# Optimization experiments

Measured on AMD Instinct MI355X. Metric: run time of the kernel, lower is better.

The kernel has to match this reference:

```python
import jax, jax.numpy as jnp
import numpy as np

N, E, D, H, C, ED = 50000, 800000, 128, 4, 32, 1
EFF = H * C  # 128 == D, so residual proj is Identity
FFN_H = 2 * EFF


def setup_inputs() -> dict:
    key = jax.random.key(0)
    ks = jax.random.split(key, 16)
    def p(k, shape, fan_in):
        return jax.random.normal(k, shape, dtype=jnp.float32) / np.sqrt(fan_in)
    return {
        "x": jax.random.normal(ks[0], (N, D), dtype=jnp.float32),
        "edge_attr": jax.random.normal(ks[1], (E, ED), dtype=jnp.float32),
        "W_l": p(ks[2], (D, EFF), D),
        "b_l": jnp.zeros((EFF,), jnp.float32),
        "W_r": p(ks[3], (D, EFF), D),
        "b_r": jnp.zeros((EFF,), jnp.float32),
        "W_e": p(ks[4], (ED, EFF), ED),
        "att": p(ks[5], (H, C), C),
        "bias_out": jnp.zeros((EFF,), jnp.float32),
        "W_gate": p(ks[6], (EFF, 1), EFF),
        "b_gate": jnp.zeros((1,), jnp.float32),
        "W_ffn1": p(ks[7], (EFF, FFN_H), EFF),
        "b_ffn1": jnp.zeros((FFN_H,), jnp.float32),
        "W_ffn2": p(ks[8], (FFN_H, EFF), FFN_H),
        "b_ffn2": jnp.zeros((EFF,), jnp.float32),
        "ln_gamma": jnp.ones((EFF,), jnp.float32),
        "ln_beta": jnp.zeros((EFF,), jnp.float32),
        "edge_index": jax.random.randint(ks[9], (2, E), 0, N, dtype=jnp.int32),
    }


def _gat_block(x, edge_attr, W_l, b_l, W_r, b_r, W_e, att, bias_out,
               W_gate, b_gate, W_ffn1, b_ffn1, W_ffn2, b_ffn2,
               ln_gamma, ln_beta, edge_index):
    n = x.shape[0]
    # add self loops (PyG default), edge_attr filled with mean
    loop = jnp.arange(n, dtype=edge_index.dtype)
    src = jnp.concatenate([edge_index[0], loop])
    dst = jnp.concatenate([edge_index[1], loop])
    ea = jnp.concatenate([edge_attr,
                          jnp.broadcast_to(edge_attr.mean(0, keepdims=True), (n, edge_attr.shape[1]))])
    # GATv2: separate source/target transforms + edge embedding
    xl = (x @ W_l + b_l).reshape(n, H, C)   # source features
    xr = (x @ W_r + b_r).reshape(n, H, C)   # target features
    ee = (ea @ W_e).reshape(-1, H, C)
    xj = xl[src]                             # [Et,H,C]
    m = jax.nn.leaky_relu(xj + xr[dst] + ee, negative_slope=0.2)
    logits = jnp.einsum('ehc,hc->eh', m, att)           # [Et,H]
    # segment softmax over destination nodes
    mx = jax.ops.segment_max(logits, dst, num_segments=n)
    ex = jnp.exp(logits - mx[dst])
    den = jax.ops.segment_sum(ex, dst, num_segments=n)
    alpha = ex / den[dst]
    out = jax.ops.segment_sum(xj * alpha[..., None], dst, num_segments=n)
    out = out.reshape(n, EFF) + bias_out
    # block: ELU, gated residual (proj is Identity since D==EFF), FFN, LayerNorm
    h = jax.nn.elu(out)
    gate = jax.nn.sigmoid(h @ W_gate + b_gate)
    y = gate * h + (1.0 - gate) * x
    ffn = jax.nn.relu(y @ W_ffn1 + b_ffn1) @ W_ffn2 + b_ffn2
    y = y + ffn
    mu = y.mean(-1, keepdims=True)
    var = y.var(-1, keepdims=True)
    y = (y - mu) * jax.lax.rsqrt(var + 1e-5) * ln_gamma + ln_beta
    return y  # dropout is identity in eval mode


def reference(x, edge_attr, W_l, b_l, W_r, b_r, W_e, att, bias_out,
              W_gate, b_gate, W_ffn1, b_ffn1, W_ffn2, b_ffn2,
              ln_gamma, ln_beta, edge_index):
    return _gat_block(x, edge_attr, W_l, b_l, W_r, b_r, W_e, att, bias_out,
                      W_gate, b_gate, W_ffn1, b_ffn1, W_ffn2, b_ffn2,
                      ln_gamma, ln_beta, edge_index)
```

## Files before the change

kernel.cpp:

```cpp
#include <hip/hip_runtime.h>
#include <hip/hip_bf16.h>

#define NODES 50000
#define NEDGE 800000
#define ETOT  850000

#define NRANGE 49
#define SB 256
#define ES ((ETOT + SB - 1) / SB)

#define XF_TILES 1563
#define HIST_BLKS 256
#define FUSE_GRID (2 * HIST_BLKS + (XF_TILES - HIST_BLKS))

typedef __hip_bfloat16 bf16;
typedef __attribute__((ext_vector_type(8))) short bf16x8;
typedef __attribute__((ext_vector_type(4))) float f32x4;

__device__ __forceinline__ bf16 f2bf(float v) { return __float2bfloat16(v); }
__device__ __forceinline__ float bflo(unsigned int v) { return __uint_as_float(v << 16); }
__device__ __forceinline__ float bfhi(unsigned int v) { return __uint_as_float(v & 0xffff0000u); }

__device__ __forceinline__ unsigned int pack2(float a, float b) {
    bf16 x = f2bf(a), y = f2bf(b);
    unsigned short xs = *reinterpret_cast<unsigned short*>(&x);
    unsigned short ys = *reinterpret_cast<unsigned short*>(&y);
    return ((unsigned int)ys << 16) | (unsigned int)xs;
}

__device__ __forceinline__ unsigned short bfbits(float v) {
    bf16 x = f2bf(v);
    return *reinterpret_cast<unsigned short*>(&x);
}

__device__ __forceinline__ void hilo(float v, unsigned short& h, unsigned short& l) {
    h = bfbits(v);
    float hv = __uint_as_float((unsigned int)h << 16);
    l = bfbits(v - hv);
}

__device__ __forceinline__ void split8(const float* v, bf16x8& hi, bf16x8& lo) {
    #pragma unroll
    for (int e = 0; e < 8; ++e) {
        unsigned short hb, lb;
        hilo(v[e], hb, lb);
        ((short*)&hi)[e] = (short)hb;
        ((short*)&lo)[e] = (short)lb;
    }
}

__global__ __launch_bounds__(256) void k_wx(const float* W_l, const float* W_r,
                                            const float* W1, const float* W2,
                                            bf16* wlh, bf16* wll,
                                            bf16* wrh, bf16* wrl,
                                            bf16* w1h, bf16* w1l,
                                            bf16* w2h, bf16* w2l) {
    int tid = blockIdx.x * blockDim.x + threadIdx.x;
    unsigned short h, l;
    if (tid < 32768) {
        int m = tid >> 14, t = tid & 16383;
        int c = t >> 7, k = t & 127;
        hilo((m ? W_r : W_l)[k * 128 + c], h, l);
        (m ? wrh : wlh)[t] = *(bf16*)&h;
        (m ? wrl : wll)[t] = *(bf16*)&l;
    } else if (tid < 65536) {
        int t = tid - 32768;
        int c = t >> 7, k = t & 127;
        hilo(W1[k * 256 + c], h, l);
        w1h[t] = *(bf16*)&h;
        w1l[t] = *(bf16*)&l;
    } else {
        int t = tid - 65536;
        int c = t >> 8, k = t & 255;
        hilo(W2[k * 128 + c], h, l);
        w2h[t] = *(bf16*)&h;
        w2l[t] = *(bf16*)&l;
    }
}

__global__ __launch_bounds__(256) void k_fuse(const float* edge_attr, const int* ei,
                                              float* sum_ea, int* rhist,
                                              const float* x,
                                              const bf16* wlh, const bf16* wll,
                                              const bf16* wrh, const bf16* wrl,
                                              const float* b_l, const float* b_r,
                                              bf16* xl, bf16* xr) {
    __shared__ __align__(16) float s_x[32][132];
    const int bid = blockIdx.x;
    int idx;
    bool isprep;
    if (bid < 2 * HIST_BLKS) { isprep = (bid & 1); idx = bid >> 1; }
    else { isprep = false; idx = HIST_BLKS + (bid - 2 * HIST_BLKS); }

    if (isprep) {
        int* hcnt = (int*)&s_x[0][0];
        const int t = threadIdx.x;
        if (t < 64) hcnt[t] = 0;
        __syncthreads();
        const int e0 = idx * ES;
        int e1 = e0 + ES; if (e1 > ETOT) e1 = ETOT;
        float local = 0.f;
        for (int e = e0 + t; e < e1; e += 256) {
            int dst = (e < NEDGE) ? ei[NEDGE + e] : (e - NEDGE);
            atomicAdd(&hcnt[dst >> 10], 1);
            if (e < NEDGE) local += edge_attr[e];
        }
        #pragma unroll
        for (int s = 1; s < 64; s <<= 1) local += __shfl_xor(local, s, 64);
        if ((t & 63) == 0) atomicAdd(sum_ea, local);
        __syncthreads();
        if (t < 64) rhist[idx * 64 + t] = hcnt[t];
        return;
    }

    const int tid = threadIdx.x;
    const int n0 = idx * 32;
    for (int it = 0; it < 4; ++it) {
        int idx4 = (it * 256 + tid) * 4;
        int n = idx4 >> 7, j = idx4 & 127;
        int node = n0 + n;
        float4 v = make_float4(0.f, 0.f, 0.f, 0.f);
        if (node < NODES) v = *(const float4*)(x + node * 128 + j);
        *(float4*)&s_x[n][j] = v;
    }
    __syncthreads();

    const int wv4  = tid >> 6;
    const int ln   = tid & 63;
    const int lrow = ln & 15;
    const int lk8  = (ln >> 4) << 3;
    const int m    = wv4 >> 1;
    const int cb   = (wv4 & 1) * 64;
    const bf16* Bh = m ? wrh : wlh;
    const bf16* Bl = m ? wrl : wll;
    const float* bias = m ? b_r : b_l;

    f32x4 acc[2][4];
    #pragma unroll
    for (int mt = 0; mt < 2; ++mt)
        #pragma unroll
        for (int i = 0; i < 4; ++i)
            acc[mt][i] = (f32x4){0.f, 0.f, 0.f, 0.f};
    #pragma unroll
    for (int kk = 0; kk < 4; ++kk) {
        int k0 = kk * 32 + lk8;
        float a0f[8], a1f[8];
        *(float4*)&a0f[0] = *(const float4*)&s_x[lrow][k0];
        *(float4*)&a0f[4] = *(const float4*)&s_x[lrow][k0 + 4];
        *(float4*)&a1f[0] = *(const float4*)&s_x[16 + lrow][k0];
        *(float4*)&a1f[4] = *(const float4*)&s_x[16 + lrow][k0 + 4];
        bf16x8 a0h, a0l, a1h, a1l;
        split8(a0f, a0h, a0l);
        split8(a1f, a1h, a1l);
        #pragma unroll
        for (int i = 0; i < 4; ++i) {
            int col = cb + (i << 4) + lrow;
            bf16x8 bh = *(const bf16x8*)(Bh + col * 128 + k0);
            bf16x8 bl = *(const bf16x8*)(Bl + col * 128 + k0);
            acc[0][i] = __builtin_amdgcn_mfma_f32_16x16x32_bf16(a0l, bh, acc[0][i], 0, 0, 0);
            acc[0][i] = __builtin_amdgcn_mfma_f32_16x16x32_bf16(a0h, bl, acc[0][i], 0, 0, 0);
            acc[0][i] = __builtin_amdgcn_mfma_f32_16x16x32_bf16(a0h, bh, acc[0][i], 0, 0, 0);
            acc[1][i] = __builtin_amdgcn_mfma_f32_16x16x32_bf16(a1l, bh, acc[1][i], 0, 0, 0);
            acc[1][i] = __builtin_amdgcn_mfma_f32_16x16x32_bf16(a1h, bl, acc[1][i], 0, 0, 0);
            acc[1][i] = __builtin_amdgcn_mfma_f32_16x16x32_bf16(a1h, bh, acc[1][i], 0, 0, 0);
        }
    }
    __syncthreads();
    bf16* s_o = (bf16*)&s_x[0][0];
    #pragma unroll
    for (int mt = 0; mt < 2; ++mt) {
        #pragma unroll
        for (int i = 0; i < 4; ++i) {
            int colg = cb + (i << 4) + lrow;
            float bv = bias[colg];
            #pragma unroll
            for (int r = 0; r < 4; ++r) {
                int row = (mt << 4) + ((ln >> 4) << 2) + r;
                s_o[row * 264 + m * 136 + colg] = f2bf(acc[mt][i][r] + bv);
            }
        }
    }
    __syncthreads();
    #pragma unroll
    for (int rep = 0; rep < 2; ++rep) {
        int idx2 = rep * 256 + tid;
        int row = idx2 >> 4, cc = (idx2 & 15) * 8;
        int node = n0 + row;
        if (node < NODES) {
            *(float4*)(xl + node * 128 + cc) = *(const float4*)(s_o + row * 264 + cc);
            *(float4*)(xr + node * 128 + cc) = *(const float4*)(s_o + row * 264 + 136 + cc);
        }
    }
}

__global__ __launch_bounds__(256) void k_rscan(int* rhist, int* base_r, int* off) {
    __shared__ int s_w[4];
    __shared__ int s_run;
    const int t = threadIdx.x, lane = t & 63, w = t >> 6;
    if (t == 0) s_run = 0;
    __syncthreads();
    for (int r = 0; r < NRANGE; ++r) {
        int v = rhist[t * 64 + r];
        int inc = v;
        #pragma unroll
        for (int d = 1; d < 64; d <<= 1) {
            int y = __shfl_up(inc, d, 64);
            if (lane >= d) inc += y;
        }
        if (lane == 63) s_w[w] = inc;
        __syncthreads();
        int woff = 0;
        #pragma unroll
        for (int ww = 0; ww < 4; ++ww) if (ww < w) woff += s_w[ww];
        int tot = s_w[0] + s_w[1] + s_w[2] + s_w[3];
        int runv = s_run;
        rhist[t * 64 + r] = runv + woff + (inc - v);
        if (t == 0) base_r[r] = runv;
        __syncthreads();
        if (t == 0) s_run = runv + tot;
        __syncthreads();
    }
    if (t == 0) { base_r[NRANGE] = ETOT; off[NODES] = ETOT; }
}

__global__ __launch_bounds__(256) void k_scatter(const int* ei, const float* edge_attr,
                                                 const float* sum_ea, const int* rhist,
                                                 uint2* tmp2) {
    __shared__ int cur[64];
    const int b = blockIdx.x, t = threadIdx.x;
    if (t < 64) cur[t] = rhist[b * 64 + t];
    __syncthreads();
    const float meanv = sum_ea[0] * (1.f / (float)NEDGE);
    const int e0 = b * ES;
    int e1 = e0 + ES; if (e1 > ETOT) e1 = ETOT;
    for (int e = e0 + t; e < e1; e += 256) {
        int src, dst; float eav;
        if (e < NEDGE) { src = ei[e]; dst = ei[NEDGE + e]; eav = edge_attr[e]; }
        else           { src = e - NEDGE; dst = src; eav = meanv; }
        int pos = atomicAdd(&cur[dst >> 10], 1);
        tmp2[pos] = make_uint2((unsigned int)dst,
                               ((unsigned int)bfbits(eav) << 16) | (unsigned int)src);
    }
}

__global__ __launch_bounds__(1024) void k_group(const uint2* tmp2, const int* base_r,
                                                int* off, unsigned int* perm) {
    __shared__ int lcnt[1024];
    __shared__ int s_w16[16];
    const int r = blockIdx.x, t = threadIdx.x;
    const int lane = t & 63, w = t >> 6;
    const int n0 = r << 10;
    const int s0 = base_r[r], s1 = base_r[r + 1];
    lcnt[t] = 0;
    __syncthreads();
    for (int i = s0 + t; i < s1; i += 1024) {
        int d = (int)tmp2[i].x;
        atomicAdd(&lcnt[d - n0], 1);
    }
    __syncthreads();
    int v = lcnt[t];
    int inc = v;
    #pragma unroll
    for (int d = 1; d < 64; d <<= 1) {
        int y = __shfl_up(inc, d, 64);
        if (lane >= d) inc += y;
    }
    if (lane == 63) s_w16[w] = inc;
    __syncthreads();
    int woff = 0;
    #pragma unroll
    for (int ww = 0; ww < 16; ++ww) if (ww < w) woff += s_w16[ww];
    int pos0 = s0 + woff + (inc - v);
    lcnt[t] = pos0;
    if (n0 + t < NODES) off[n0 + t] = pos0;
    __syncthreads();
    for (int i = s0 + t; i < s1; i += 1024) {
        uint2 p = tmp2[i];
        int pos = atomicAdd(&lcnt[(int)p.x - n0], 1);
        perm[pos] = p.y;
    }
}

__global__ __launch_bounds__(256) void k_agge(const unsigned int* xl32,
                                              const unsigned int* xr32,
                                              const unsigned int* perm, const int* off,
                                              const float* W_e, const float* att,
                                              const float* bias_out,
                                              const float* x,
                                              const float* W_gate, const float* b_gate,
                                              const bf16* w1h, const bf16* w1l,
                                              const float* b_ffn1,
                                              const bf16* w2h, const bf16* w2l,
                                              const float* b_ffn2,
                                              const float* gamma, const float* beta,
                                              float* out) {
    __shared__ __align__(16) float s_y[32][132];
    __shared__ __align__(16) float s_t[32][260];
    __shared__ float s_g[32];
    __shared__ float s_mu[32], s_rs[32];
    const int tid = threadIdx.x;
    const int lane = tid & 63;
    const int wvi  = tid >> 6;
    const int n0 = blockIdx.x * 32;
    int nn = NODES - n0; if (nn > 32) nn = 32;

    {
        const int c = 2 * lane;
        const float we1 = W_e[c], we2 = W_e[c + 1];
        const float a1 = att[c], a2 = att[c + 1];
        const float bo1 = bias_out[c], bo2 = bias_out[c + 1];
        for (int s = 0; s < 8; ++s) {
            const int nl = wvi * 8 + s;
            const int n = n0 + nl;
            if (n < NODES) {
                unsigned int xru = xr32[n * 64 + lane];
                float xr1 = bflo(xru), xr2 = bfhi(xru);
                int s0 = off[n], s1 = off[n + 1];
                float m = -1e30f, l = 0.f, acc1 = 0.f, acc2 = 0.f;
                int j = s0;
                for (; j + 4 <= s1; j += 4) {
                    unsigned int u0 = perm[j];
                    unsigned int u1 = perm[j + 1];
                    unsigned int u2 = perm[j + 2];
                    unsigned int u3 = perm[j + 3];
                    unsigned int g0 = xl32[(u0 & 0xffffu) * 64 + lane];
                    unsigned int g1 = xl32[(u1 & 0xffffu) * 64 + lane];
                    unsigned int g2 = xl32[(u2 & 0xffffu) * 64 + lane];
                    unsigned int g3 = xl32[(u3 & 0xffffu) * 64 + lane];
                    float e0 = bfhi(u0), e1 = bfhi(u1), e2 = bfhi(u2), e3 = bfhi(u3);
                    float x01 = bflo(g0), x02 = bfhi(g0);
                    float x11 = bflo(g1), x12 = bfhi(g1);
                    float x21 = bflo(g2), x22 = bfhi(g2);
                    float x31 = bflo(g3), x32 = bfhi(g3);
                    float p0, p1, p2, p3;
                    {
                        float v1 = x01 + xr1 + e0 * we1, v2 = x02 + xr2 + e0 * we2;
                        v1 = (v1 > 0.f) ? v1 : 0.2f * v1;
                        v2 = (v2 > 0.f) ? v2 : 0.2f * v2;
                        p0 = v1 * a1 + v2 * a2;
                    }
                    {
                        float v1 = x11 + xr1 + e1 * we1, v2 = x12 + xr2 + e1 * we2;
                        v1 = (v1 > 0.f) ? v1 : 0.2f * v1;
                        v2 = (v2 > 0.f) ? v2 : 0.2f * v2;
                        p1 = v1 * a1 + v2 * a2;
                    }
                    {
                        float v1 = x21 + xr1 + e2 * we1, v2 = x22 + xr2 + e2 * we2;
                        v1 = (v1 > 0.f) ? v1 : 0.2f * v1;
                        v2 = (v2 > 0.f) ? v2 : 0.2f * v2;
                        p2 = v1 * a1 + v2 * a2;
                    }
                    {
                        float v1 = x31 + xr1 + e3 * we1, v2 = x32 + xr2 + e3 * we2;
                        v1 = (v1 > 0.f) ? v1 : 0.2f * v1;
                        v2 = (v2 > 0.f) ? v2 : 0.2f * v2;
                        p3 = v1 * a1 + v2 * a2;
                    }
                    p0 += __shfl_xor(p0, 1, 64); p1 += __shfl_xor(p1, 1, 64);
                    p2 += __shfl_xor(p2, 1, 64); p3 += __shfl_xor(p3, 1, 64);
                    p0 += __shfl_xor(p0, 2, 64); p1 += __shfl_xor(p1, 2, 64);
                    p2 += __shfl_xor(p2, 2, 64); p3 += __shfl_xor(p3, 2, 64);
                    p0 += __shfl_xor(p0, 4, 64); p1 += __shfl_xor(p1, 4, 64);
                    p2 += __shfl_xor(p2, 4, 64); p3 += __shfl_xor(p3, 4, 64);
                    p0 += __shfl_xor(p0, 8, 64); p1 += __shfl_xor(p1, 8, 64);
                    p2 += __shfl_xor(p2, 8, 64); p3 += __shfl_xor(p3, 8, 64);
                    float nm = fmaxf(fmaxf(m, fmaxf(p0, p1)), fmaxf(p2, p3));
                    float sc = __expf(m - nm);
                    float E0 = __expf(p0 - nm);
                    float E1 = __expf(p1 - nm);
                    float E2 = __expf(p2 - nm);
                    float E3 = __expf(p3 - nm);
                    l = l * sc + E0 + E1 + E2 + E3;
                    acc1 = acc1 * sc + E0 * x01 + E1 * x11 + E2 * x21 + E3 * x31;
                    acc2 = acc2 * sc + E0 * x02 + E1 * x12 + E2 * x22 + E3 * x32;
                    m = nm;
                }
                for (; j < s1; ++j) {
                    unsigned int u0 = perm[j];
                    unsigned int g0 = xl32[(u0 & 0xffffu) * 64 + lane];
                    float e0 = bfhi(u0);
                    float x01 = bflo(g0), x02 = bfhi(g0);
                    float v1 = x01 + xr1 + e0 * we1, v2 = x02 + xr2 + e0 * we2;
                    v1 = (v1 > 0.f) ? v1 : 0.2f * v1;
                    v2 = (v2 > 0.f) ? v2 : 0.2f * v2;
                    float p = v1 * a1 + v2 * a2;
                    p += __shfl_xor(p, 1, 64);
                    p += __shfl_xor(p, 2, 64);
                    p += __shfl_xor(p, 4, 64);
                    p += __shfl_xor(p, 8, 64);
                    float nm = fmaxf(m, p);
                    float sc = __expf(m - nm);
                    float ee = __expf(p - nm);
                    l = l * sc + ee;
                    acc1 = acc1 * sc + ee * x01;
                    acc2 = acc2 * sc + ee * x02;
                    m = nm;
                }
                float inv = 1.f / fmaxf(l, 1e-30f);
                float r1 = acc1 * inv + bo1;
                float r2 = acc2 * inv + bo2;
                r1 = (r1 > 0.f) ? r1 : (__expf(r1) - 1.f);
                r2 = (r2 > 0.f) ? r2 : (__expf(r2) - 1.f);
                *(float2*)&s_y[nl][c] = make_float2(r1, r2);
            } else {
                *(float2*)&s_y[nl][c] = make_float2(0.f, 0.f);
            }
        }
    }
    __syncthreads();
    {
        int n = tid >> 3, kb = (tid & 7) * 16;
        float g = 0.f;
        #pragma unroll
        for (int k = 0; k < 16; k += 4) {
            float4 w = *(const float4*)(W_gate + kb + k);
            float4 h = *(const float4*)&s_y[n][kb + k];
            g += h.x * w.x + h.y * w.y + h.z * w.z + h.w * w.w;
        }
        g += __shfl_xor(g, 1, 64);
        g += __shfl_xor(g, 2, 64);
        g += __shfl_xor(g, 4, 64);
        if ((tid & 7) == 0) s_g[n] = 1.f / (1.f + __expf(-(g + b_gate[0])));
    }
    __syncthreads();
    for (int it = 0; it < 4; ++it) {
        int idx4 = (it * 256 + tid) * 4;
        int n = idx4 >> 7, j = idx4 & 127;
        if (n < nn) {
            float g = s_g[n];
            float4 xv = *(const float4*)(x + (n0 + n) * 128 + j);
            float4 h = *(float4*)&s_y[n][j];
            h.x = g * h.x + (1.f - g) * xv.x;
            h.y = g * h.y + (1.f - g) * xv.y;
            h.z = g * h.z + (1.f - g) * xv.z;
            h.w = g * h.w + (1.f - g) * xv.w;
            *(float4*)&s_y[n][j] = h;
        }
    }
    __syncthreads();

    const int wv   = wvi;
    const int ln   = lane;
    const int lrow = ln & 15;
    const int lk8  = (ln >> 4) << 3;

    f32x4 acc1[2][4];
    #pragma unroll
    for (int mt = 0; mt < 2; ++mt)
        #pragma unroll
        for (int i = 0; i < 4; ++i)
            acc1[mt][i] = (f32x4){0.f, 0.f, 0.f, 0.f};
    #pragma unroll
    for (int kk = 0; kk < 4; ++kk) {
        int k0 = kk * 32 + lk8;
        float a0f[8], a1f[8];
        *(float4*)&a0f[0] = *(const float4*)&s_y[lrow][k0];
        *(float4*)&a0f[4] = *(const float4*)&s_y[lrow][k0 + 4];
        *(float4*)&a1f[0] = *(const float4*)&s_y[16 + lrow][k0];
        *(float4*)&a1f[4] = *(const float4*)&s_y[16 + lrow][k0 + 4];
        bf16x8 a0h, a0l, a1h, a1l;
        split8(a0f, a0h, a0l);
        split8(a1f, a1h, a1l);
        #pragma unroll
        for (int i = 0; i < 4; ++i) {
            int col = (wv << 6) + (i << 4) + lrow;
            bf16x8 bh = *(const bf16x8*)(w1h + col * 128 + k0);
            bf16x8 bl = *(const bf16x8*)(w1l + col * 128 + k0);
            acc1[0][i] = __builtin_amdgcn_mfma_f32_16x16x32_bf16(a0l, bh, acc1[0][i], 0, 0, 0);
            acc1[0][i] = __builtin_amdgcn_mfma_f32_16x16x32_bf16(a0h, bl, acc1[0][i], 0, 0, 0);
            acc1[0][i] = __builtin_amdgcn_mfma_f32_16x16x32_bf16(a0h, bh, acc1[0][i], 0, 0, 0);
            acc1[1][i] = __builtin_amdgcn_mfma_f32_16x16x32_bf16(a1l, bh, acc1[1][i], 0, 0, 0);
            acc1[1][i] = __builtin_amdgcn_mfma_f32_16x16x32_bf16(a1h, bl, acc1[1][i], 0, 0, 0);
            acc1[1][i] = __builtin_amdgcn_mfma_f32_16x16x32_bf16(a1h, bh, acc1[1][i], 0, 0, 0);
        }
    }
    #pragma unroll
    for (int mt = 0; mt < 2; ++mt) {
        #pragma unroll
        for (int i = 0; i < 4; ++i) {
            int col = (wv << 6) + (i << 4) + lrow;
            float bv = b_ffn1[col];
            #pragma unroll
            for (int r = 0; r < 4; ++r) {
                int row = (mt << 4) + ((ln >> 4) << 2) + r;
                s_t[row][col] = fmaxf(acc1[mt][i][r] + bv, 0.f);
            }
        }
    }
    __syncthreads();

    f32x4 acc2[2][2];
    #pragma unroll
    for (int mt = 0; mt < 2; ++mt)
        #pragma unroll
        for (int c = 0; c < 2; ++c)
            acc2[mt][c] = (f32x4){0.f, 0.f, 0.f, 0.f};
    #pragma unroll
    for (int kk = 0; kk < 8; ++kk) {
        int k0 = kk * 32 + lk8;
        float a0f[8], a1f[8];
        *(float4*)&a0f[0] = *(const float4*)&s_t[lrow][k0];
        *(float4*)&a0f[4] = *(const float4*)&s_t[lrow][k0 + 4];
        *(float4*)&a1f[0] = *(const float4*)&s_t[16 + lrow][k0];
        *(float4*)&a1f[4] = *(const float4*)&s_t[16 + lrow][k0 + 4];
        bf16x8 a0h, a0l, a1h, a1l;
        split8(a0f, a0h, a0l);
        split8(a1f, a1h, a1l);
        #pragma unroll
        for (int c = 0; c < 2; ++c) {
            int col = (wv << 5) + (c << 4) + lrow;
            bf16x8 bh = *(const bf16x8*)(w2h + col * 256 + k0);
            bf16x8 bl = *(const bf16x8*)(w2l + col * 256 + k0);
            acc2[0][c] = __builtin_amdgcn_mfma_f32_16x16x32_bf16(a0l, bh, acc2[0][c], 0, 0, 0);
            acc2[0][c] = __builtin_amdgcn_mfma_f32_16x16x32_bf16(a0h, bl, acc2[0][c], 0, 0, 0);
            acc2[0][c] = __builtin_amdgcn_mfma_f32_16x16x32_bf16(a0h, bh, acc2[0][c], 0, 0, 0);
            acc2[1][c] = __builtin_amdgcn_mfma_f32_16x16x32_bf16(a1l, bh, acc2[1][c], 0, 0, 0);
            acc2[1][c] = __builtin_amdgcn_mfma_f32_16x16x32_bf16(a1h, bl, acc2[1][c], 0, 0, 0);
            acc2[1][c] = __builtin_amdgcn_mfma_f32_16x16x32_bf16(a1h, bh, acc2[1][c], 0, 0, 0);
        }
    }
    #pragma unroll
    for (int mt = 0; mt < 2; ++mt) {
        #pragma unroll
        for (int c = 0; c < 2; ++c) {
            int col = (wv << 5) + (c << 4) + lrow;
            float bv = b_ffn2[col];
            #pragma unroll
            for (int r = 0; r < 4; ++r) {
                int row = (mt << 4) + ((ln >> 4) << 2) + r;
                s_y[row][col] += acc2[mt][c][r] + bv;
            }
        }
    }
    __syncthreads();
    {
        int n = tid >> 3, kb = (tid & 7) * 16;
        float s = 0.f, ss = 0.f;
        #pragma unroll
        for (int k = 0; k < 16; k += 4) {
            float4 v = *(const float4*)&s_y[n][kb + k];
            s  += v.x + v.y + v.z + v.w;
            ss += v.x * v.x + v.y * v.y + v.z * v.z + v.w * v.w;
        }
        s  += __shfl_xor(s, 1, 64);  ss += __shfl_xor(ss, 1, 64);
        s  += __shfl_xor(s, 2, 64);  ss += __shfl_xor(ss, 2, 64);
        s  += __shfl_xor(s, 4, 64);  ss += __shfl_xor(ss, 4, 64);
        if ((tid & 7) == 0) {
            float mu = s * (1.f / 128.f);
            float var = ss * (1.f / 128.f) - mu * mu;
            s_mu[n] = mu;
            s_rs[n] = rsqrtf(fmaxf(var, 0.f) + 1e-5f);
        }
    }
    __syncthreads();
    for (int it = 0; it < 4; ++it) {
        int idx4 = (it * 256 + tid) * 4;
        int n = idx4 >> 7, j = idx4 & 127;
        if (n < nn) {
            float mu = s_mu[n], rs = s_rs[n];
            float4 gv = *(const float4*)(gamma + j);
            float4 bv = *(const float4*)(beta + j);
            float4 v = *(const float4*)&s_y[n][j];
            float4 o;
            o.x = (v.x - mu) * rs * gv.x + bv.x;
            o.y = (v.y - mu) * rs * gv.y + bv.y;
            o.z = (v.z - mu) * rs * gv.z + bv.z;
            o.w = (v.w - mu) * rs * gv.w + bv.w;
            *(float4*)(out + (n0 + n) * 128 + j) = o;
        }
    }
}

extern "C" void kernel_launch(void* const* d_in, const int* in_sizes, int n_in,
                              void* d_out, int out_size, void* d_ws, size_t ws_size,
                              hipStream_t stream) {
    const float* x         = (const float*)d_in[0];
    const float* edge_attr = (const float*)d_in[1];
    const int* edge_index  = (const int*)d_in[17];
    float* out = (float*)d_out;

    char* base = (char*)d_ws;
    float* sum_ea  = (float*)(base + 16);
    int*   rhist   = (int*)  (base + 32);
    bf16*  w1t_hi  = (bf16*) (base + 32 + 65536);
    bf16*  w1t_lo  = (bf16*) (base + 32 + 131072);
    int*   off     = (int*)  (base + 200032);
    int*   base_r  = (int*)  (base + 400064);
    bf16*  w2t_hi  = (bf16*) (base + 400064 + 256);
    bf16*  w2t_lo  = (bf16*) (base + 400064 + 256 + 65536);
    unsigned int* perm = (unsigned int*)(base + 600064);
    bf16*  xl      = (bf16*) (base + 4000064);
    bf16*  xr      = (bf16*) (base + 16800064);
    bf16*  wxlh    = (bf16*) (base + 600064 + 1024);
    bf16*  wxll    = (bf16*) (base + 600064 + 1024 + 32768);
    bf16*  wxrh    = (bf16*) (base + 600064 + 1024 + 65536);
    bf16*  wxrl    = (bf16*) (base + 600064 + 1024 + 98304);
    uint2* tmp2    = (uint2*)d_out;

    hipMemsetAsync(sum_ea, 0, 16, stream);

    const int NTILES = (NODES + 31) / 32;

    k_wx      <<<384, 256, 0, stream>>>((const float*)d_in[2], (const float*)d_in[4],
                                        (const float*)d_in[11], (const float*)d_in[13],
                                        wxlh, wxll, wxrh, wxrl,
                                        w1t_hi, w1t_lo, w2t_hi, w2t_lo);
    k_fuse    <<<FUSE_GRID, 256, 0, stream>>>(edge_attr, edge_index, sum_ea, rhist,
                                              x, wxlh, wxll, wxrh, wxrl,
                                              (const float*)d_in[3], (const float*)d_in[5],
                                              xl, xr);
    k_rscan   <<<1, 256, 0, stream>>>(rhist, base_r, off);
    k_scatter <<<SB, 256, 0, stream>>>(edge_index, edge_attr, sum_ea, rhist, tmp2);
    k_group   <<<NRANGE, 1024, 0, stream>>>(tmp2, base_r, off, perm);
    k_agge    <<<NTILES, 256, 0, stream>>>((const unsigned int*)xl,
                                           (const unsigned int*)xr,
                                           perm, off,
                                           (const float*)d_in[6], (const float*)d_in[7],
                                           (const float*)d_in[8], x,
                                           (const float*)d_in[9], (const float*)d_in[10],
                                           w1t_hi, w1t_lo, (const float*)d_in[12],
                                           w2t_hi, w2t_lo, (const float*)d_in[14],
                                           (const float*)d_in[15], (const float*)d_in[16],
                                           out);
}
```

Measured before the change: 391.3 us.

## Split fused aggregation+FFN kernel into separate aggregation and epilogue kernels

The fused gather/softmax-aggregation plus gate/FFN/LayerNorm kernel is split in two. A lightweight aggregation kernel uses a wave-per-node grid-stride loop with no LDS, so more waves can be resident to hide gather latency. Its results go to global memory, and an epilogue kernel reads them back. The gate dot product is now computed per wave with shuffles instead of extra LDS passes. This adds a 25.6 MB fp32 round trip through global memory and one more launch, in exchange for higher occupancy on the latency-bound gather.

```diff
diff --git a/kernel.cpp b/kernel.cpp
--- a/kernel.cpp
+++ b/kernel.cpp
@@ -281,22 +281,118 @@
     }
 }
 
-__global__ __launch_bounds__(256) void k_agge(const unsigned int* xl32,
-                                              const unsigned int* xr32,
-                                              const unsigned int* perm, const int* off,
-                                              const float* W_e, const float* att,
-                                              const float* bias_out,
-                                              const float* x,
-                                              const float* W_gate, const float* b_gate,
-                                              const bf16* w1h, const bf16* w1l,
-                                              const float* b_ffn1,
-                                              const bf16* w2h, const bf16* w2l,
-                                              const float* b_ffn2,
-                                              const float* gamma, const float* beta,
-                                              float* out) {
+__global__ __launch_bounds__(256) void k_agg(const unsigned int* xl32,
+                                             const unsigned int* xr32,
+                                             const unsigned int* perm, const int* off,
+                                             const float* W_e, const float* att,
+                                             float* outp) {
+    const int lane = threadIdx.x & 63;
+    const int wave0 = blockIdx.x * 4 + (threadIdx.x >> 6);
+    const int nwaves = gridDim.x * 4;
+    const int c = 2 * lane;
+    const float we1 = W_e[c], we2 = W_e[c + 1];
+    const float a1 = att[c], a2 = att[c + 1];
+    for (int n = wave0; n < NODES; n += nwaves) {
+        unsigned int xru = xr32[n * 64 + lane];
+        float xr1 = bflo(xru), xr2 = bfhi(xru);
+        int s0 = off[n], s1 = off[n + 1];
+        float m = -1e30f, l = 0.f, acc1 = 0.f, acc2 = 0.f;
+        int j = s0;
+        for (; j + 4 <= s1; j += 4) {
+            unsigned int u0 = perm[j];
+            unsigned int u1 = perm[j + 1];
+            unsigned int u2 = perm[j + 2];
+            unsigned int u3 = perm[j + 3];
+            unsigned int g0 = xl32[(u0 & 0xffffu) * 64 + lane];
+            unsigned int g1 = xl32[(u1 & 0xffffu) * 64 + lane];
+            unsigned int g2 = xl32[(u2 & 0xffffu) * 64 + lane];
+            unsigned int g3 = xl32[(u3 & 0xffffu) * 64 + lane];
+            float e0 = bfhi(u0), e1 = bfhi(u1), e2 = bfhi(u2), e3 = bfhi(u3);
+            float x01 = bflo(g0), x02 = bfhi(g0);
+            float x11 = bflo(g1), x12 = bfhi(g1);
+            float x21 = bflo(g2), x22 = bfhi(g2);
+            float x31 = bflo(g3), x32 = bfhi(g3);
+            float p0, p1, p2, p3;
+            {
+                float v1 = x01 + xr1 + e0 * we1, v2 = x02 + xr2 + e0 * we2;
+                v1 = (v1 > 0.f) ? v1 : 0.2f * v1;
+                v2 = (v2 > 0.f) ? v2 : 0.2f * v2;
+                p0 = v1 * a1 + v2 * a2;
+            }
+            {
+                float v1 = x11 + xr1 + e1 * we1, v2 = x12 + xr2 + e1 * we2;
+                v1 = (v1 > 0.f) ? v1 : 0.2f * v1;
+                v2 = (v2 > 0.f) ? v2 : 0.2f * v2;
+                p1 = v1 * a1 + v2 * a2;
+            }
+            {
+                float v1 = x21 + xr1 + e2 * we1, v2 = x22 + xr2 + e2 * we2;
+                v1 = (v1 > 0.f) ? v1 : 0.2f * v1;
+                v2 = (v2 > 0.f) ? v2 : 0.2f * v2;
+                p2 = v1 * a1 + v2 * a2;
+            }
+            {
+                float v1 = x31 + xr1 + e3 * we1, v2 = x32 + xr2 + e3 * we2;
+                v1 = (v1 > 0.f) ? v1 : 0.2f * v1;
+                v2 = (v2 > 0.f) ? v2 : 0.2f * v2;
+                p3 = v1 * a1 + v2 * a2;
+            }
+            p0 += __shfl_xor(p0, 1, 64); p1 += __shfl_xor(p1, 1, 64);
+            p2 += __shfl_xor(p2, 1, 64); p3 += __shfl_xor(p3, 1, 64);
+            p0 += __shfl_xor(p0, 2, 64); p1 += __shfl_xor(p1, 2, 64);
+            p2 += __shfl_xor(p2, 2, 64); p3 += __shfl_xor(p3, 2, 64);
+            p0 += __shfl_xor(p0, 4, 64); p1 += __shfl_xor(p1, 4, 64);
+            p2 += __shfl_xor(p2, 4, 64); p3 += __shfl_xor(p3, 4, 64);
+            p0 += __shfl_xor(p0, 8, 64); p1 += __shfl_xor(p1, 8, 64);
+            p2 += __shfl_xor(p2, 8, 64); p3 += __shfl_xor(p3, 8, 64);
+            float nm = fmaxf(fmaxf(m, fmaxf(p0, p1)), fmaxf(p2, p3));
+            float sc = __expf(m - nm);
+            float E0 = __expf(p0 - nm);
+            float E1 = __expf(p1 - nm);
+            float E2 = __expf(p2 - nm);
+            float E3 = __expf(p3 - nm);
+            l = l * sc + E0 + E1 + E2 + E3;
+            acc1 = acc1 * sc + E0 * x01 + E1 * x11 + E2 * x21 + E3 * x31;
+            acc2 = acc2 * sc + E0 * x02 + E1 * x12 + E2 * x22 + E3 * x32;
+            m = nm;
+        }
+        for (; j < s1; ++j) {
+            unsigned int u0 = perm[j];
+            unsigned int g0 = xl32[(u0 & 0xffffu) * 64 + lane];
+            float e0 = bfhi(u0);
+            float x01 = bflo(g0), x02 = bfhi(g0);
+            float v1 = x01 + xr1 + e0 * we1, v2 = x02 + xr2 + e0 * we2;
+            v1 = (v1 > 0.f) ? v1 : 0.2f * v1;
+            v2 = (v2 > 0.f) ? v2 : 0.2f * v2;
+            float p = v1 * a1 + v2 * a2;
+            p += __shfl_xor(p, 1, 64);
+            p += __shfl_xor(p, 2, 64);
+            p += __shfl_xor(p, 4, 64);
+            p += __shfl_xor(p, 8, 64);
+            float nm = fmaxf(m, p);
+            float sc = __expf(m - nm);
+            float ee = __expf(p - nm);
+            l = l * sc + ee;
+            acc1 = acc1 * sc + ee * x01;
+            acc2 = acc2 * sc + ee * x02;
+            m = nm;
+        }
+        float inv = 1.f / fmaxf(l, 1e-30f);
+        *(float2*)(outp + n * 128 + c) = make_float2(acc1 * inv, acc2 * inv);
+    }
+}
+
+__global__ __launch_bounds__(256) void k_epi(const float* out_agg, const float* x,
+                                             const float* bias_out,
+                                             const float* W_gate, const float* b_gate,
+                                             const bf16* w1h, const bf16* w1l,
+                                             const float* b_ffn1,
+                                             const bf16* w2h, const bf16* w2l,
+                                             const float* b_ffn2,
+                                             const float* gamma, const float* beta,
+                                             float* out) {
     __shared__ __align__(16) float s_y[32][132];
     __shared__ __align__(16) float s_t[32][260];
-    __shared__ float s_g[32];
     __shared__ float s_mu[32], s_rs[32];
     const int tid = threadIdx.x;
     const int lane = tid & 63;
@@ -306,136 +402,32 @@
 
     {
         const int c = 2 * lane;
-        const float we1 = W_e[c], we2 = W_e[c + 1];
-        const float a1 = att[c], a2 = att[c + 1];
-        const float bo1 = bias_out[c], bo2 = bias_out[c + 1];
+        const float bo1 = bias_out[c],  bo2 = bias_out[c + 1];
+        const float wg1 = W_gate[c],    wg2 = W_gate[c + 1];
+        const float bg0 = b_gate[0];
         for (int s = 0; s < 8; ++s) {
             const int nl = wvi * 8 + s;
             const int n = n0 + nl;
             if (n < NODES) {
-                unsigned int xru = xr32[n * 64 + lane];
-                float xr1 = bflo(xru), xr2 = bfhi(xru);
-                int s0 = off[n], s1 = off[n + 1];
-                float m = -1e30f, l = 0.f, acc1 = 0.f, acc2 = 0.f;
-                int j = s0;
-                for (; j + 4 <= s1; j += 4) {
-                    unsigned int u0 = perm[j];
-                    unsigned int u1 = perm[j + 1];
-                    unsigned int u2 = perm[j + 2];
-                    unsigned int u3 = perm[j + 3];
-                    unsigned int g0 = xl32[(u0 & 0xffffu) * 64 + lane];
-                    unsigned int g1 = xl32[(u1 & 0xffffu) * 64 + lane];
-                    unsigned int g2 = xl32[(u2 & 0xffffu) * 64 + lane];
-                    unsigned int g3 = xl32[(u3 & 0xffffu) * 64 + lane];
-                    float e0 = bfhi(u0), e1 = bfhi(u1), e2 = bfhi(u2), e3 = bfhi(u3);
-                    float x01 = bflo(g0), x02 = bfhi(g0);
-                    float x11 = bflo(g1), x12 = bfhi(g1);
-                    float x21 = bflo(g2), x22 = bfhi(g2);
-                    float x31 = bflo(g3), x32 = bfhi(g3);
-                    float p0, p1, p2, p3;
-                    {
-                        float v1 = x01 + xr1 + e0 * we1, v2 = x02 + xr2 + e0 * we2;
-                        v1 = (v1 > 0.f) ? v1 : 0.2f * v1;
-                        v2 = (v2 > 0.f) ? v2 : 0.2f * v2;
-                        p0 = v1 * a1 + v2 * a2;
-                    }
-                    {
-                        float v1 = x11 + xr1 + e1 * we1, v2 = x12 + xr2 + e1 * we2;
-                        v1 = (v1 > 0.f) ? v1 : 0.2f * v1;
-                        v2 = (v2 > 0.f) ? v2 : 0.2f * v2;
-                        p1 = v1 * a1 + v2 * a2;
-                    }
-                    {
-                        float v1 = x21 + xr1 + e2 * we1, v2 = x22 + xr2 + e2 * we2;
-                        v1 = (v1 > 0.f) ? v1 : 0.2f * v1;
-                        v2 = (v2 > 0.f) ? v2 : 0.2f * v2;
-                        p2 = v1 * a1 + v2 * a2;
-                    }
-                    {
-                        float v1 = x31 + xr1 + e3 * we1, v2 = x32 + xr2 + e3 * we2;
-                        v1 = (v1 > 0.f) ? v1 : 0.2f * v1;
-                        v2 = (v2 > 0.f) ? v2 : 0.2f * v2;
-                        p3 = v1 * a1 + v2 * a2;
-                    }
-                    p0 += __shfl_xor(p0, 1, 64); p1 += __shfl_xor(p1, 1, 64);
-                    p2 += __shfl_xor(p2, 1, 64); p3 += __shfl_xor(p3, 1, 64);
-                    p0 += __shfl_xor(p0, 2, 64); p1 += __shfl_xor(p1, 2, 64);
-                    p2 += __shfl_xor(p2, 2, 64); p3 += __shfl_xor(p3, 2, 64);
-                    p0 += __shfl_xor(p0, 4, 64); p1 += __shfl_xor(p1, 4, 64);
-                    p2 += __shfl_xor(p2, 4, 64); p3 += __shfl_xor(p3, 4, 64);
-                    p0 += __shfl_xor(p0, 8, 64); p1 += __shfl_xor(p1, 8, 64);
-                    p2 += __shfl_xor(p2, 8, 64); p3 += __shfl_xor(p3, 8, 64);
-                    float nm = fmaxf(fmaxf(m, fmaxf(p0, p1)), fmaxf(p2, p3));
-                    float sc = __expf(m - nm);
-                    float E0 = __expf(p0 - nm);
-                    float E1 = __expf(p1 - nm);
-                    float E2 = __expf(p2 - nm);
-                    float E3 = __expf(p3 - nm);
-                    l = l * sc + E0 + E1 + E2 + E3;
-                    acc1 = acc1 * sc + E0 * x01 + E1 * x11 + E2 * x21 + E3 * x31;
-                    acc2 = acc2 * sc + E0 * x02 + E1 * x12 + E2 * x22 + E3 * x32;
-                    m = nm;
-                }
-                for (; j < s1; ++j) {
-                    unsigned int u0 = perm[j];
-                    unsigned int g0 = xl32[(u0 & 0xffffu) * 64 + lane];
-                    float e0 = bfhi(u0);
-                    float x01 = bflo(g0), x02 = bfhi(g0);
-                    float v1 = x01 + xr1 + e0 * we1, v2 = x02 + xr2 + e0 * we2;
-                    v1 = (v1 > 0.f) ? v1 : 0.2f * v1;
-                    v2 = (v2 > 0.f) ? v2 : 0.2f * v2;
-                    float p = v1 * a1 + v2 * a2;
-                    p += __shfl_xor(p, 1, 64);
-                    p += __shfl_xor(p, 2, 64);
-                    p += __shfl_xor(p, 4, 64);
-                    p += __shfl_xor(p, 8, 64);
-                    float nm = fmaxf(m, p);
-                    float sc = __expf(m - nm);
-                    float ee = __expf(p - nm);
-                    l = l * sc + ee;
-                    acc1 = acc1 * sc + ee * x01;
-                    acc2 = acc2 * sc + ee * x02;
-                    m = nm;
-                }
-                float inv = 1.f / fmaxf(l, 1e-30f);
-                float r1 = acc1 * inv + bo1;
-                float r2 = acc2 * inv + bo2;
-                r1 = (r1 > 0.f) ? r1 : (__expf(r1) - 1.f);
-                r2 = (r2 > 0.f) ? r2 : (__expf(r2) - 1.f);
-                *(float2*)&s_y[nl][c] = make_float2(r1, r2);
+                float2 v = *(const float2*)(out_agg + n * 128 + c);
+                float h1 = v.x + bo1, h2 = v.y + bo2;
+                h1 = (h1 > 0.f) ? h1 : (__expf(h1) - 1.f);
+                h2 = (h2 > 0.f) ? h2 : (__expf(h2) - 1.f);
+                float g = h1 * wg1 + h2 * wg2;
+                g += __shfl_xor(g, 1, 64);
+                g += __shfl_xor(g, 2, 64);
+                g += __shfl_xor(g, 4, 64);
+                g += __shfl_xor(g, 8, 64);
+                g += __shfl_xor(g, 16, 64);
+                g += __shfl_xor(g, 32, 64);
+                g = 1.f / (1.f + __expf(-(g + bg0)));
+                float2 xv = *(const float2*)(x + n * 128 + c);
+                float y1 = g * h1 + (1.f - g) * xv.x;
+                float y2 = g * h2 + (1.f - g) * xv.y;
+                *(float2*)&s_y[nl][c] = make_float2(y1, y2);
             } else {
                 *(float2*)&s_y[nl][c] = make_float2(0.f, 0.f);
             }
-        }
-    }
-    __syncthreads();
-    {
-        int n = tid >> 3, kb = (tid & 7) * 16;
-        float g = 0.f;
-        #pragma unroll
-        for (int k = 0; k < 16; k += 4) {
-            float4 w = *(const float4*)(W_gate + kb + k);
-            float4 h = *(const float4*)&s_y[n][kb + k];
-            g += h.x * w.x + h.y * w.y + h.z * w.z + h.w * w.w;
-        }
-        g += __shfl_xor(g, 1, 64);
-        g += __shfl_xor(g, 2, 64);
-        g += __shfl_xor(g, 4, 64);
-        if ((tid & 7) == 0) s_g[n] = 1.f / (1.f + __expf(-(g + b_gate[0])));
-    }
-    __syncthreads();
-    for (int it = 0; it < 4; ++it) {
-        int idx4 = (it * 256 + tid) * 4;
-        int n = idx4 >> 7, j = idx4 & 127;
-        if (n < nn) {
-            float g = s_g[n];
-            float4 xv = *(const float4*)(x + (n0 + n) * 128 + j);
-            float4 h = *(float4*)&s_y[n][j];
-            h.x = g * h.x + (1.f - g) * xv.x;
-            h.y = g * h.y + (1.f - g) * xv.y;
-            h.z = g * h.z + (1.f - g) * xv.z;
-            h.w = g * h.w + (1.f - g) * xv.w;
-            *(float4*)&s_y[n][j] = h;
         }
     }
     __syncthreads();
@@ -613,11 +605,12 @@
     k_rscan   <<<1, 256, 0, stream>>>(rhist, base_r, off);
     k_scatter <<<SB, 256, 0, stream>>>(edge_index, edge_attr, sum_ea, rhist, tmp2);
     k_group   <<<NRANGE, 1024, 0, stream>>>(tmp2, base_r, off, perm);
-    k_agge    <<<NTILES, 256, 0, stream>>>((const unsigned int*)xl,
-                                           (const unsigned int*)xr,
-                                           perm, off,
-                                           (const float*)d_in[6], (const float*)d_in[7],
-                                           (const float*)d_in[8], x,
+    k_agg     <<<3125, 256, 0, stream>>>((const unsigned int*)xl,
+                                         (const unsigned int*)xr,
+                                         perm, off,
+                                         (const float*)d_in[6], (const float*)d_in[7],
+                                         out);
+    k_epi     <<<NTILES, 256, 0, stream>>>(out, x, (const float*)d_in[8],
                                            (const float*)d_in[9], (const float*)d_in[10],
                                            w1t_hi, w1t_lo, (const float*)d_in[12],
                                            w2t_hi, w2t_lo, (const float*)d_in[14],
```

Result: faster. 349.9 us (-10.6%).
